# Optimization experiments

Measured on AMD Instinct MI355X. Metric: run time of the kernel, lower is better.

The kernel has to match this reference:

```python
import jax, jax.numpy as jnp
import numpy as np

BETA = 0.99
TOL = 1e-4
MAX_ITER = 1000
EPS = 1e-3
B, N, HF, HV, KV = 65536, 32, 25, 128, 8


def fhat(x, fp):
    W1, b1, W2, b2, W3, b3 = fp
    h = jax.nn.softplus(x @ W1 + b1)
    h = jax.nn.softplus(h @ W2 + b2)
    return h @ W3 + b3  # (B,1,N)


def V(z, vp):
    # Lyapunov function: V(z) = ||g(z)-g(0)||^2 + eps*||z||^2 ; V(0)=0, V>0 elsewhere.
    W1, b1, W2, b2, W3, b3 = vp
    def mlp(u):
        h = jax.nn.softplus(u @ W1 + b1)
        h = jax.nn.softplus(h @ W2 + b2)
        return h @ W3 + b3
    h = mlp(z)
    h0 = mlp(jnp.zeros((1, 1, z.shape[-1]), z.dtype))
    return (jnp.sum((h - h0) ** 2, axis=-1, keepdims=True)
            + EPS * jnp.sum(z * z, axis=-1, keepdims=True))  # (B,1,1)


def newton_F(fhatx, target, gamma, vp):
    # F = gamma - (V(fhatx*gamma)-target)/dV_dgamma  (newton_iter.forward)
    Vg, dV = jax.jvp(lambda g: V(fhatx * g, vp), (gamma,), (jnp.ones_like(gamma),))
    return gamma - (Vg - target) / dV


def solve_gamma(fhatx, target, vp):
    # Vectorized masked Newton + bisection (rootfind_train.forward).
    gamma = jnp.ones((fhatx.shape[0], 1, 1), fhatx.dtype)
    e1 = jnp.zeros_like(gamma)
    e2 = jnp.ones_like(gamma)
    active = (V(fhatx, vp) - target) > 0.0  # samples needing rootfind

    def cond(s):
        return jnp.logical_and(jnp.any(s[3]), s[4] < MAX_ITER)

    def body(s):
        gamma, e1, e2, m, it = s
        # Newton step on active, unconverged samples
        newt = newton_F(fhatx, target, gamma, vp)
        gamma = jnp.where(m, newt, gamma)
        # bisection backup where Newton left [e1,e2] (or produced non-finite)
        m_bisec = m & ((gamma < e1) | (gamma > e2) | ~jnp.isfinite(gamma))
        a = 0.5 * (e1 + e2)
        s_a = jnp.sign(V(fhatx * a, vp) - target)
        s_1 = jnp.sign(V(fhatx * e1, vp) - target)
        s_2 = jnp.sign(V(fhatx * e2, vp) - target)
        e2 = jnp.where(m_bisec & (s_a * s_1 < 0), a, e2)
        e1 = jnp.where(m_bisec & (s_a * s_2 < 0), a, e1)
        gamma = jnp.where(m_bisec, a, gamma)
        m = active & (jnp.abs(V(fhatx * gamma, vp) - target) > TOL)
        return (gamma, e1, e2, m, it + 1)

    gamma = jax.lax.while_loop(cond, body, (gamma, e1, e2, active, jnp.int32(0)))[0]
    return gamma


@jax.jit
def _forward(x, fp, vp):
    fhatx = fhat(x, fp)
    target = BETA * V(x, vp)
    viol = V(fhatx, vp) > target  # these go through rootfind; rest pass through fhat
    gamma = solve_gamma(fhatx, target, vp)
    return jnp.where(viol, fhatx * gamma, fhatx)


def setup_inputs() -> dict:
    key = jax.random.key(0)
    ks = jax.random.split(key, 13)
    def w(k, shape, fan):
        return jax.random.normal(k, shape, jnp.float32) / np.float32(np.sqrt(fan))
    return {
        'x': jax.random.normal(ks[0], (B, 1, N), jnp.float32),
        'f_W1': w(ks[1], (N, HF), N), 'f_b1': jnp.zeros((HF,), jnp.float32),
        'f_W2': w(ks[2], (HF, HF), HF), 'f_b2': jnp.zeros((HF,), jnp.float32),
        'f_W3': w(ks[3], (HF, N), HF), 'f_b3': jnp.zeros((N,), jnp.float32),
        'v_W1': w(ks[4], (N, HV), N), 'v_b1': jnp.zeros((HV,), jnp.float32),
        'v_W2': w(ks[5], (HV, HV), HV), 'v_b2': jnp.zeros((HV,), jnp.float32),
        'v_W3': w(ks[6], (HV, KV), HV), 'v_b3': jnp.zeros((KV,), jnp.float32),
    }


def reference(x, f_W1, f_b1, f_W2, f_b2, f_W3, f_b3,
              v_W1, v_b1, v_W2, v_b2, v_W3, v_b3):
    fp = (f_W1, f_b1, f_W2, f_b2, f_W3, f_b3)
    vp = (v_W1, v_b1, v_W2, v_b2, v_W3, v_b3)
    return _forward(x, fp, vp)
```

## Files before the change

### kernel.cpp

```cpp
#include <hip/hip_runtime.h>
#include <math.h>

#define BETA_C   0.99f
#define TOL_C    1e-4f
#define ACC_C    1e-3f
#define BRK_C    1e-3f
#define FORCE_C  6
#define MAXIT_C  1000
#define EPS_C    1e-3f
#define BN       65536
#define NN       32
#define HFD      25
#define HVD      128
#define KVD      8
#define G        16
#define GPB      16
#define SGPB     16
#define SBLK     256
#define NQBLK    1024

typedef __attribute__((ext_vector_type(8))) short bf16x8;
typedef __attribute__((ext_vector_type(8))) unsigned short u16x8;
typedef __attribute__((ext_vector_type(4))) float f32x4;

__device__ __forceinline__ void wsync() {
    __builtin_amdgcn_wave_barrier();
    __threadfence_block();
    __builtin_amdgcn_wave_barrier();
}

__device__ __forceinline__ float sp_(float x) {
    return fmaxf(x, 0.f) + log1pf(expf(-fabsf(x)));
}
__device__ __forceinline__ float spf_(float x) {
    return fmaxf(x, 0.f) + __logf(1.f + __expf(-fabsf(x)));
}
__device__ __forceinline__ float sgn_(float d) {
    return (d > 0.f) ? 1.f : ((d < 0.f) ? -1.f : 0.f);
}
__device__ __forceinline__ unsigned short f2bf(float f) {
    unsigned int u = __float_as_uint(f);
    u += 0x7FFFu + ((u >> 16) & 1u);
    return (unsigned short)(u >> 16);
}
__device__ __forceinline__ float bf2f(unsigned short u) {
    return __uint_as_float(((unsigned int)u) << 16);
}

__device__ __forceinline__ void aw_st(unsigned short* aw, int row, int col, float v) {
    const int b = (row * 64 + col * 2) ^ ((row & 3) << 4);
    *(unsigned short*)((char*)aw + b) = f2bf(v);
}
__device__ __forceinline__ bf16x8 aw_ld(const unsigned short* aw, int row, int k) {
    const int b = (row * 64 + k * 2) ^ ((row & 3) << 4);
    return *(const bf16x8*)((const char*)aw + b);
}
__device__ __forceinline__ void hw_st(unsigned short* hw, int row, int col, float v) {
    const int b = (row * 256 + col * 2) ^ ((row & 7) << 4);
    *(unsigned short*)((char*)hw + b) = f2bf(v);
}
__device__ __forceinline__ bf16x8 hw_ld(const unsigned short* hw, int row, int k) {
    const int b = (row * 256 + k * 2) ^ ((row & 7) << 4);
    return *(const bf16x8*)((const char*)hw + b);
}

__device__ __forceinline__ void veval2_sec(
    const int gl, const float (&uA)[8], const float (&uB)[8],
    const float gA, const float gB,
    float2* h1q, const float n2A, const float n2B,
    const float (&b1v)[8], const float (&b2v)[8], const float (&d0c)[8],
    const unsigned short* w2L, const unsigned short* w3L,
    float& VA, float& VB)
{
    const int k0 = gl * 8;
#pragma unroll
    for (int j = 0; j < 8; ++j) {
        const float preA = fmaf(gA, uA[j], b1v[j]);
        const float preB = fmaf(gB, uB[j], b1v[j]);
        h1q[k0 + j] = make_float2(spf_(preA), spf_(preB));
    }
    wsync();
    float aA[8], aB[8];
#pragma unroll
    for (int j = 0; j < 8; ++j) { aA[j] = 0.f; aB[j] = 0.f; }
#pragma unroll 4
    for (int k = 0; k < HVD; ++k) {
        const float2 q = h1q[k];
        const u16x8 wv = *(const u16x8*)(w2L + k * HVD + k0);
#pragma unroll
        for (int j = 0; j < 8; ++j) {
            const float w = bf2f(wv[j]);
            aA[j] = fmaf(q.x, w, aA[j]);
            aB[j] = fmaf(q.y, w, aB[j]);
        }
    }
    wsync();
    float oA[KVD], oB[KVD];
#pragma unroll
    for (int c = 0; c < KVD; ++c) { oA[c] = 0.f; oB[c] = 0.f; }
#pragma unroll
    for (int j = 0; j < 8; ++j) {
        const float h2A = spf_(aA[j] + b2v[j]);
        const float h2B = spf_(aB[j] + b2v[j]);
        const u16x8 w3v = *(const u16x8*)(w3L + (k0 + j) * KVD);
#pragma unroll
        for (int c = 0; c < 8; ++c) {
            const float w3 = bf2f(w3v[c]);
            oA[c] = fmaf(h2A, w3, oA[c]);
            oB[c] = fmaf(h2B, w3, oB[c]);
        }
    }
#pragma unroll
    for (int m = 1; m < G; m <<= 1) {
#pragma unroll
        for (int c = 0; c < KVD; ++c) {
            oA[c] += __shfl_xor(oA[c], m);
            oB[c] += __shfl_xor(oB[c], m);
        }
    }
    float vvA = 0.f, vvB = 0.f;
#pragma unroll
    for (int c = 0; c < KVD; ++c) {
        const float eA = oA[c] + d0c[c];
        const float eB = oB[c] + d0c[c];
        vvA = fmaf(eA, eA, vvA);
        vvB = fmaf(eB, eB, vvB);
    }
    VA = vvA + EPS_C * gA * gA * n2A;
    VB = vvB + EPS_C * gB * gB * n2B;
}

__global__ __launch_bounds__(128) void k_h0(
    const float* __restrict__ vb1, const float* __restrict__ vW2,
    const float* __restrict__ vb2, const float* __restrict__ vW3,
    const float* __restrict__ vb3, float* __restrict__ h0g)
{
    __shared__ float h1s[HVD];
    __shared__ float h2s[HVD];
    int j = threadIdx.x;
    h1s[j] = sp_(vb1[j]);
    __syncthreads();
    float a = vb2[j];
    for (int k = 0; k < HVD; ++k) a = fmaf(h1s[k], vW2[k * HVD + j], a);
    h2s[j] = sp_(a);
    __syncthreads();
    if (j < KVD) {
        float acc = vb3[j];
        for (int k = 0; k < HVD; ++k) acc = fmaf(h2s[k], vW3[k * KVD + j], acc);
        h0g[j] = acc;
    }
}

__global__ __launch_bounds__(256) void k_wprep(
    const float* __restrict__ vW1, const float* __restrict__ vW2,
    const float* __restrict__ vW3,
    unsigned short* __restrict__ w1b, unsigned short* __restrict__ w2b,
    unsigned short* __restrict__ w3b,
    unsigned short* __restrict__ w2s, unsigned short* __restrict__ w3s)
{
    const int t = blockIdx.x * 256 + threadIdx.x;
    const int nth = gridDim.x * 256;
    for (int i = t; i < HVD * NN; i += nth) {
        const int col = i >> 5, k = i & 31;
        w1b[i] = f2bf(vW1[k * HVD + col]);
    }
    for (int i = t; i < HVD * HVD; i += nth) {
        const int col = i >> 7, k = i & 127;
        w2b[i] = f2bf(vW2[k * HVD + col]);
    }
    for (int i = t; i < 16 * HVD; i += nth) {
        const int c = i >> 7, k = i & 127;
        w3b[i] = (c < KVD) ? f2bf(vW3[k * KVD + c]) : (unsigned short)0;
    }
    for (int i = t; i < HVD * HVD; i += nth)
        w2s[i] = f2bf(vW2[i]);
    for (int i = t; i < HVD * KVD; i += nth)
        w3s[i] = f2bf(vW3[i]);
}

__global__ __launch_bounds__(256, 4) void k_setup(
    const float* __restrict__ x_g,
    const float* __restrict__ fW1, const float* __restrict__ fb1,
    const float* __restrict__ fW2, const float* __restrict__ fb2,
    const float* __restrict__ fW3, const float* __restrict__ fb3,
    const float* __restrict__ vb1, const float* __restrict__ vb2,
    const float* __restrict__ vb3,
    const unsigned short* __restrict__ w1b,
    const unsigned short* __restrict__ w2b,
    const unsigned short* __restrict__ w3b,
    const float* __restrict__ h0g,
    float* __restrict__ out,
    int* __restrict__ cnt, int* __restrict__ list, float* __restrict__ tgt,
    float* __restrict__ vfb)
{
    __shared__ float2 xs[GPB][NN + 1];
    __shared__ float fh1[GPB][HFD + 1];
    __shared__ float fh2[GPB][HFD + 1];
    __shared__ __align__(16) unsigned short abf[4][16 * 32];
    __shared__ __align__(16) unsigned short hbf[4][16 * HVD];
    __shared__ int wcnt[4];
    __shared__ int bbase;

    const int tid = threadIdx.x;
    const int gi = tid >> 4;
    const int gl = tid & (G - 1);
    const int w  = tid >> 6;
    const int l  = tid & 63;
    const int q  = l >> 4;
    const int cc = l & 15;
    const int sb = (blockIdx.x * GPB + gi) * 2;
    const int s0 = sb, s1 = sb + 1;
    unsigned short* aw = abf[w];
    unsigned short* hw = hbf[w];

    const float xa0 = x_g[(size_t)s0 * NN + gl];
    const float xa1 = x_g[(size_t)s0 * NN + gl + 16];
    const float xb0 = x_g[(size_t)s1 * NN + gl];
    const float xb1 = x_g[(size_t)s1 * NN + gl + 16];
    xs[gi][gl]      = make_float2(xa0, xb0);
    xs[gi][gl + 16] = make_float2(xa1, xb1);
    const int r0 = 4 * q;
    aw_st(aw, r0,     gl,      xa0); aw_st(aw, r0,     gl + 16, xa1);
    aw_st(aw, r0 + 2, gl,      xb0); aw_st(aw, r0 + 2, gl + 16, xb1);
    wsync();

    float fA0, fA1, fB0, fB1;
#pragma unroll
    for (int si = 0; si < 2; ++si) {
        for (int uu = gl; uu < HFD; uu += G) {
            float a = fb1[uu];
#pragma unroll
            for (int i = 0; i < NN; ++i) {
                const float2 xv2 = xs[gi][i];
                const float xv = si ? xv2.y : xv2.x;
                a = fmaf(xv, fW1[i * HFD + uu], a);
            }
            fh1[gi][uu] = spf_(a);
        }
        wsync();
        for (int uu = gl; uu < HFD; uu += G) {
            float a = fb2[uu];
#pragma unroll
            for (int i = 0; i < HFD; ++i)
                a = fmaf(fh1[gi][i], fW2[i * HFD + uu], a);
            fh2[gi][uu] = spf_(a);
        }
        wsync();
        float fo0 = fb3[gl], fo1 = fb3[gl + 16];
#pragma unroll
        for (int i = 0; i < HFD; ++i) {
            const float h = fh2[gi][i];
            fo0 = fmaf(h, fW3[i * NN + gl], fo0);
            fo1 = fmaf(h, fW3[i * NN + gl + 16], fo1);
        }
        const int ss = si ? s1 : s0;
        out[(size_t)ss * NN + gl]      = fo0;
        out[(size_t)ss * NN + gl + 16] = fo1;
        aw_st(aw, r0 + 1 + 2 * si, gl,      fo0);
        aw_st(aw, r0 + 1 + 2 * si, gl + 16, fo1);
        if (si == 0) { fA0 = fo0; fA1 = fo1; } else { fB0 = fo0; fB1 = fo1; }
        wsync();
    }

    float p0 = fmaf(xa0, xa0, xa1 * xa1);
    float p1 = fmaf(fA0, fA0, fA1 * fA1);
    float p2 = fmaf(xb0, xb0, xb1 * xb1);
    float p3 = fmaf(fB0, fB0, fB1 * fB1);
#pragma unroll
    for (int m = 1; m < G; m <<= 1) {
        p0 += __shfl_xor(p0, m); p1 += __shfl_xor(p1, m);
        p2 += __shfl_xor(p2, m); p3 += __shfl_xor(p3, m);
    }

    float b1v[8], b2v[8];
#pragma unroll
    for (int n = 0; n < 8; ++n) {
        b1v[n] = vb1[n * 16 + cc];
        b2v[n] = vb2[n * 16 + cc];
    }

    const int kq = (l >> 4) * 8;
    const f32x4 zf = {0.f, 0.f, 0.f, 0.f};

    const bf16x8 afr = aw_ld(aw, cc, kq);
    f32x4 acc1[8];
#pragma unroll
    for (int n = 0; n < 8; ++n) {
        const bf16x8 bfr = *(const bf16x8*)(w1b + (n * 16 + cc) * 32 + kq);
        acc1[n] = __builtin_amdgcn_mfma_f32_16x16x32_bf16(afr, bfr, zf, 0, 0, 0);
    }
#pragma unroll
    for (int n = 0; n < 8; ++n) {
#pragma unroll
        for (int r = 0; r < 4; ++r)
            hw_st(hw, r0 + r, n * 16 + cc, spf_(acc1[n][r] + b1v[n]));
    }
    wsync();

    f32x4 acc2[8];
#pragma unroll
    for (int n = 0; n < 8; ++n) acc2[n] = zf;
#pragma unroll
    for (int c = 0; c < 4; ++c) {
        const bf16x8 a2f = hw_ld(hw, cc, c * 32 + kq);
#pragma unroll
        for (int n = 0; n < 8; ++n) {
            const bf16x8 b2f = *(const bf16x8*)(w2b + (n * 16 + cc) * HVD + c * 32 + kq);
            acc2[n] = __builtin_amdgcn_mfma_f32_16x16x32_bf16(a2f, b2f, acc2[n], 0, 0, 0);
        }
    }
    wsync();
#pragma unroll
    for (int n = 0; n < 8; ++n) {
#pragma unroll
        for (int r = 0; r < 4; ++r)
            hw_st(hw, r0 + r, n * 16 + cc, spf_(acc2[n][r] + b2v[n]));
    }
    wsync();

    f32x4 acc3 = zf;
#pragma unroll
    for (int c = 0; c < 4; ++c) {
        const bf16x8 a3f = hw_ld(hw, cc, c * 32 + kq);
        const bf16x8 b3f = *(const bf16x8*)(w3b + cc * HVD + c * 32 + kq);
        acc3 = __builtin_amdgcn_mfma_f32_16x16x32_bf16(a3f, b3f, acc3, 0, 0, 0);
    }

    const float d0 = (cc < KVD) ? (vb3[cc] - h0g[cc]) : 0.f;
    float s_[4];
#pragma unroll
    for (int r = 0; r < 4; ++r) {
        const float e = (cc < KVD) ? (acc3[r] + d0) : 0.f;
        s_[r] = e * e;
    }
#pragma unroll
    for (int m = 1; m < G; m <<= 1) {
#pragma unroll
        for (int r = 0; r < 4; ++r) s_[r] += __shfl_xor(s_[r], m);
    }
    const float Vx0 = s_[0] + EPS_C * p0;
    const float Vf0 = s_[1] + EPS_C * p1;
    const float Vx1 = s_[2] + EPS_C * p2;
    const float Vf1 = s_[3] + EPS_C * p3;

    const float t0 = BETA_C * Vx0;
    const float t1 = BETA_C * Vx1;
    const bool act0 = (Vf0 - t0) > 0.f;
    const bool act1 = (Vf1 - t1) > 0.f;

    const bool lead = (gl == 0 && act0) || (gl == 1 && act1);
    unsigned long long bal = __ballot(lead);
    const int lane = threadIdx.x & 63, wv = threadIdx.x >> 6;
    const int rank = __popcll(bal & ((1ull << lane) - 1ull));
    if (lane == 0) wcnt[wv] = __popcll(bal);
    __syncthreads();
    if (threadIdx.x == 0) {
        int tot = 0;
        for (int i = 0; i < 4; ++i) { int c = wcnt[i]; wcnt[i] = tot; tot += c; }
        bbase = atomicAdd(cnt, tot);
    }
    __syncthreads();
    if (lead) {
        const int p = bbase + wcnt[wv] + rank;
        list[p] = (gl == 0) ? s0 : s1;
        tgt[p]  = (gl == 0) ? t0 : t1;
        vfb[p]  = (gl == 0) ? Vf0 : Vf1;
    }
}

__global__ __launch_bounds__(SBLK, 2) void k_solve(
    const float* __restrict__ vW1, const float* __restrict__ vb1,
    const unsigned short* __restrict__ w2s, const float* __restrict__ vb2,
    const unsigned short* __restrict__ w3s, const float* __restrict__ vb3,
    const float* __restrict__ h0g,
    float* __restrict__ out,
    const int* __restrict__ cnt, const int* __restrict__ list,
    const float* __restrict__ tgt, const float* __restrict__ vfb,
    int* __restrict__ qhead)
{
    __shared__ __align__(16) unsigned short w2L[HVD * HVD];
    __shared__ __align__(16) unsigned short w3L[HVD * KVD];
    __shared__ __align__(8) float2 h1s[SGPB][HVD];
    __shared__ __align__(8) float2 fxs[SGPB][NN];

    {
        const uint4* s2 = (const uint4*)w2s;
        uint4* d2 = (uint4*)w2L;
        for (int i = threadIdx.x; i < (HVD * HVD) / 8; i += SBLK) d2[i] = s2[i];
        const uint4* s3 = (const uint4*)w3s;
        uint4* d3 = (uint4*)w3L;
        for (int i = threadIdx.x; i < (HVD * KVD) / 8; i += SBLK) d3[i] = s3[i];
    }
    __syncthreads();

    const int gi = threadIdx.x >> 4;
    const int gl = threadIdx.x & (G - 1);
    const int n  = *cnt;
    float2* h1q = h1s[gi];
    float2* fxr = fxs[gi];
    const int lead = threadIdx.x & 48;

    const int k0 = gl * 8;
    float b1v[8], b2v[8], d0c[8];
    {
        const float4 a = *(const float4*)(vb1 + k0);
        const float4 b = *(const float4*)(vb1 + k0 + 4);
        b1v[0]=a.x; b1v[1]=a.y; b1v[2]=a.z; b1v[3]=a.w;
        b1v[4]=b.x; b1v[5]=b.y; b1v[6]=b.z; b1v[7]=b.w;
        const float4 c = *(const float4*)(vb2 + k0);
        const float4 d = *(const float4*)(vb2 + k0 + 4);
        b2v[0]=c.x; b2v[1]=c.y; b2v[2]=c.z; b2v[3]=c.w;
        b2v[4]=d.x; b2v[5]=d.y; b2v[6]=d.z; b2v[7]=d.w;
#pragma unroll
        for (int cix = 0; cix < KVD; ++cix) d0c[cix] = vb3[cix] - h0g[cix];
    }

    int sA, sB; float tgA, tgB, fA0, fA1, fB0, fB1, n2A, n2B;
    float uA[8], uB[8];
    float gA, e1A, e2A, vA1, vA2, pgA, pvA;
    float gB, e1B, e2B, vB1, vB2, pgB, pvB;
    bool doneA, doneB;
    int itA, itB, obhA, obhB;

    auto grab = [&]() -> bool {
        int v = 0;
        if (gl == 0) v = atomicAdd(qhead, 2);
        v = __shfl(v, lead);
        if (v >= n) return false;
        const bool hasB = (v + 1) < n;
        sA = list[v]; tgA = tgt[v];
        const float vfA = vfb[v];
        float vfB;
        if (hasB) { sB = list[v + 1]; tgB = tgt[v + 1]; vfB = vfb[v + 1]; }
        else      { sB = sA;          tgB = tgA;        vfB = vfA; }
        fA0 = out[(size_t)sA * NN + gl];
        fA1 = out[(size_t)sA * NN + gl + 16];
        fB0 = out[(size_t)sB * NN + gl];
        fB1 = out[(size_t)sB * NN + gl + 16];
        fxr[gl]      = make_float2(fA0, fB0);
        fxr[gl + 16] = make_float2(fA1, fB1);
        wsync();
        n2A = 0.f; n2B = 0.f;
#pragma unroll
        for (int i = 0; i < NN; ++i) {
            const float2 q = fxr[i];
            n2A = fmaf(q.x, q.x, n2A);
            n2B = fmaf(q.y, q.y, n2B);
        }
#pragma unroll
        for (int j = 0; j < 8; ++j) { uA[j] = 0.f; uB[j] = 0.f; }
#pragma unroll
        for (int i = 0; i < NN; ++i) {
            const float2 q = fxr[i];
            const float4 wa = *(const float4*)(vW1 + i * HVD + k0);
            const float4 wb = *(const float4*)(vW1 + i * HVD + k0 + 4);
            uA[0] = fmaf(q.x, wa.x, uA[0]); uA[1] = fmaf(q.x, wa.y, uA[1]);
            uA[2] = fmaf(q.x, wa.z, uA[2]); uA[3] = fmaf(q.x, wa.w, uA[3]);
            uA[4] = fmaf(q.x, wb.x, uA[4]); uA[5] = fmaf(q.x, wb.y, uA[5]);
            uA[6] = fmaf(q.x, wb.z, uA[6]); uA[7] = fmaf(q.x, wb.w, uA[7]);
            uB[0] = fmaf(q.y, wa.x, uB[0]); uB[1] = fmaf(q.y, wa.y, uB[1]);
            uB[2] = fmaf(q.y, wa.z, uB[2]); uB[3] = fmaf(q.y, wa.w, uB[3]);
            uB[4] = fmaf(q.y, wb.x, uB[4]); uB[5] = fmaf(q.y, wb.y, uB[5]);
            uB[6] = fmaf(q.y, wb.z, uB[6]); uB[7] = fmaf(q.y, wb.w, uB[7]);
        }
        gA = sqrtf(tgA / vfA); e1A = 0.f; e2A = 1.f; vA1 = 0.f; vA2 = vfA;
        pgA = 1.f; pvA = vfA;
        gB = sqrtf(tgB / vfB); e1B = 0.f; e2B = 1.f; vB1 = 0.f; vB2 = vfB;
        pgB = 1.f; pvB = vfB;
        doneA = false; itA = 0; obhA = 0;
        doneB = !hasB; itB = 0; obhB = 0;
        return true;
    };
    if (!grab()) return;

    auto step = [&](bool& done, float& gamma, float& pg, float& pv,
                    float& e1, float& e2, float& v_e1, float& v_e2,
                    int& it, int& obh,
                    const float vp, const float target,
                    const int s, const float f0, const float f1) {
        if (done) return;
        if (fabsf(vp - target) <= TOL_C || (e2 - e1) <= BRK_C) {
            out[(size_t)s * NN + gl]      = f0 * gamma;
            out[(size_t)s * NN + gl + 16] = f1 * gamma;
            done = true;
            return;
        }
        const float sa = sgn_(vp - target);
        const float s1 = sgn_(v_e1 - target);
        if (sa * s1 < 0.f) { e2 = gamma; v_e2 = vp; }
        else               { e1 = gamma; v_e1 = vp; }
        ++it;
        const float newt = gamma - (vp - target) * (gamma - pg) / (vp - pv);
        pg = gamma; pv = vp;
        if (it < FORCE_C && newt >= e1 && newt <= e2) {
            if (fabsf(newt - gamma) <= ACC_C) {
                out[(size_t)s * NN + gl]      = f0 * newt;
                out[(size_t)s * NN + gl + 16] = f1 * newt;
                done = true;
                return;
            }
            gamma = newt;
        } else if (newt > e2 && e2 >= 1.0f) {
            if (++obh >= 2) {
                out[(size_t)s * NN + gl]      = f0;
                out[(size_t)s * NN + gl + 16] = f1;
                done = true;
                return;
            }
            gamma = 0.5f * (e1 + e2);
        } else {
            gamma = 0.5f * (e1 + e2);
        }
        if (it >= MAXIT_C) {
            out[(size_t)s * NN + gl]      = f0 * gamma;
            out[(size_t)s * NN + gl + 16] = f1 * gamma;
            done = true;
        }
    };

    for (;;) {
        float vpA, vpB;
        veval2_sec(gl, uA, uB, gA, gB, h1q, n2A, n2B,
                   b1v, b2v, d0c, w2L, w3L, vpA, vpB);
        step(doneA, gA, pgA, pvA, e1A, e2A, vA1, vA2, itA, obhA, vpA, tgA, sA, fA0, fA1);
        step(doneB, gB, pgB, pvB, e1B, e2B, vB1, vB2, itB, obhB, vpB, tgB, sB, fB0, fB1);
        if (doneA && doneB) {
            if (!grab()) break;
        }
    }
}

extern "C" void kernel_launch(void* const* d_in, const int* in_sizes, int n_in,
                              void* d_out, int out_size, void* d_ws, size_t ws_size,
                              hipStream_t stream)
{
    const float* x   = (const float*)d_in[0];
    const float* fW1 = (const float*)d_in[1];
    const float* fb1 = (const float*)d_in[2];
    const float* fW2 = (const float*)d_in[3];
    const float* fb2 = (const float*)d_in[4];
    const float* fW3 = (const float*)d_in[5];
    const float* fb3 = (const float*)d_in[6];
    const float* vW1 = (const float*)d_in[7];
    const float* vb1 = (const float*)d_in[8];
    const float* vW2 = (const float*)d_in[9];
    const float* vb2 = (const float*)d_in[10];
    const float* vW3 = (const float*)d_in[11];
    const float* vb3 = (const float*)d_in[12];
    float* out = (float*)d_out;

    char* ws = (char*)d_ws;
    int*   cnt   = (int*)ws;
    int*   qhead = (int*)(ws + 4);
    float* h0g   = (float*)(ws + 64);
    int*   list  = (int*)(ws + 128);
    float* tgt   = (float*)(ws + 128 + (size_t)BN * 4);
    float* vfb   = (float*)(ws + 128 + (size_t)BN * 8);
    unsigned short* w1b = (unsigned short*)(ws + 128 + (size_t)BN * 12);
    unsigned short* w2b = w1b + HVD * NN;
    unsigned short* w3b = w2b + HVD * HVD;
    unsigned short* w2s = w3b + 16 * HVD;
    unsigned short* w3s = w2s + HVD * HVD;

    hipMemsetAsync(ws, 0, 8, stream);

    hipLaunchKernelGGL(k_h0, dim3(1), dim3(HVD), 0, stream,
                       vb1, vW2, vb2, vW3, vb3, h0g);

    hipLaunchKernelGGL(k_wprep, dim3(32), dim3(256), 0, stream,
                       vW1, vW2, vW3, w1b, w2b, w3b, w2s, w3s);

    hipLaunchKernelGGL(k_setup, dim3(BN / (GPB * 2)), dim3(256), 0, stream,
                       x, fW1, fb1, fW2, fb2, fW3, fb3,
                       vb1, vb2, vb3, w1b, w2b, w3b,
                       h0g, out, cnt, list, tgt, vfb);

    hipLaunchKernelGGL(k_solve, dim3(NQBLK), dim3(SBLK), 0, stream,
                       vW1, vb1, w2s, vb2, w3s, vb3,
                       h0g, out, cnt, list, tgt, vfb, qhead);
}
```

Before: 309.1 us.

## Pack hidden activations as bf16 pairs, drop W3 LDS copy, use shuffles for inputs

The solve kernel now stores layer-1 activations as packed bf16 pairs in a transposed LDS layout, halving that buffer. It also drops the W3 and fx shared-memory copies, reading W3 straight from global memory and broadcasting input features with wave shuffles. The aim is less LDS traffic and footprint, which may allow more resident blocks. The setup kernel fuses its two per-sample f-MLP passes into one loop that handles both samples together, with fewer syncs. Rounding activations to bf16 adds precision loss in the Newton/bisection V evaluations, which could change convergence and iteration counts.

After: 444.4 us. 43.8% more time.

```diff
diff --git a/kernel.cpp b/kernel.cpp
--- a/kernel.cpp
+++ b/kernel.cpp
@@ -67,9 +67,9 @@
 __device__ __forceinline__ void veval2_sec(
     const int gl, const float (&uA)[8], const float (&uB)[8],
     const float gA, const float gB,
-    float2* h1q, const float n2A, const float n2B,
+    unsigned* h1q, const float n2A, const float n2B,
     const float (&b1v)[8], const float (&b2v)[8], const float (&d0c)[8],
-    const unsigned short* w2L, const unsigned short* w3L,
+    const unsigned short* w2L, const unsigned short* __restrict__ w3s,
     float& VA, float& VB)
 {
     const int k0 = gl * 8;
@@ -77,7 +77,9 @@
     for (int j = 0; j < 8; ++j) {
         const float preA = fmaf(gA, uA[j], b1v[j]);
         const float preB = fmaf(gB, uB[j], b1v[j]);
-        h1q[k0 + j] = make_float2(spf_(preA), spf_(preB));
+        const unsigned pa = f2bf(spf_(preA));
+        const unsigned pb = f2bf(spf_(preB));
+        h1q[(j << 4) | gl] = pa | (pb << 16);
     }
     wsync();
     float aA[8], aB[8];
@@ -85,13 +87,15 @@
     for (int j = 0; j < 8; ++j) { aA[j] = 0.f; aB[j] = 0.f; }
 #pragma unroll 4
     for (int k = 0; k < HVD; ++k) {
-        const float2 q = h1q[k];
+        const unsigned hp = h1q[((k & 7) << 4) | (k >> 3)];
+        const float qx = bf2f((unsigned short)(hp & 0xffffu));
+        const float qy = bf2f((unsigned short)(hp >> 16));
         const u16x8 wv = *(const u16x8*)(w2L + k * HVD + k0);
 #pragma unroll
         for (int j = 0; j < 8; ++j) {
             const float w = bf2f(wv[j]);
-            aA[j] = fmaf(q.x, w, aA[j]);
-            aB[j] = fmaf(q.y, w, aB[j]);
+            aA[j] = fmaf(qx, w, aA[j]);
+            aB[j] = fmaf(qy, w, aB[j]);
         }
     }
     wsync();
@@ -102,7 +106,7 @@
     for (int j = 0; j < 8; ++j) {
         const float h2A = spf_(aA[j] + b2v[j]);
         const float h2B = spf_(aB[j] + b2v[j]);
-        const u16x8 w3v = *(const u16x8*)(w3L + (k0 + j) * KVD);
+        const u16x8 w3v = *(const u16x8*)(w3s + (k0 + j) * KVD);
 #pragma unroll
         for (int c = 0; c < 8; ++c) {
             const float w3 = bf2f(w3v[c]);
@@ -194,8 +198,8 @@
     float* __restrict__ vfb)
 {
     __shared__ float2 xs[GPB][NN + 1];
-    __shared__ float fh1[GPB][HFD + 1];
-    __shared__ float fh2[GPB][HFD + 1];
+    __shared__ float2 fh1[GPB][HFD + 1];
+    __shared__ float2 fh2[GPB][HFD + 1];
     __shared__ __align__(16) unsigned short abf[4][16 * 32];
     __shared__ __align__(16) unsigned short hbf[4][16 * HVD];
     __shared__ int wcnt[4];
@@ -225,42 +229,52 @@
     wsync();
 
     float fA0, fA1, fB0, fB1;
-#pragma unroll
-    for (int si = 0; si < 2; ++si) {
-        for (int uu = gl; uu < HFD; uu += G) {
-            float a = fb1[uu];
-#pragma unroll
-            for (int i = 0; i < NN; ++i) {
-                const float2 xv2 = xs[gi][i];
-                const float xv = si ? xv2.y : xv2.x;
-                a = fmaf(xv, fW1[i * HFD + uu], a);
-            }
-            fh1[gi][uu] = spf_(a);
-        }
-        wsync();
-        for (int uu = gl; uu < HFD; uu += G) {
-            float a = fb2[uu];
-#pragma unroll
-            for (int i = 0; i < HFD; ++i)
-                a = fmaf(fh1[gi][i], fW2[i * HFD + uu], a);
-            fh2[gi][uu] = spf_(a);
-        }
-        wsync();
-        float fo0 = fb3[gl], fo1 = fb3[gl + 16];
+    for (int uu = gl; uu < HFD; uu += G) {
+        float a0 = fb1[uu];
+        float a1 = a0;
+#pragma unroll
+        for (int i = 0; i < NN; ++i) {
+            const float2 xv2 = xs[gi][i];
+            const float wv = fW1[i * HFD + uu];
+            a0 = fmaf(xv2.x, wv, a0);
+            a1 = fmaf(xv2.y, wv, a1);
+        }
+        fh1[gi][uu] = make_float2(spf_(a0), spf_(a1));
+    }
+    wsync();
+    for (int uu = gl; uu < HFD; uu += G) {
+        float a0 = fb2[uu];
+        float a1 = a0;
 #pragma unroll
         for (int i = 0; i < HFD; ++i) {
-            const float h = fh2[gi][i];
-            fo0 = fmaf(h, fW3[i * NN + gl], fo0);
-            fo1 = fmaf(h, fW3[i * NN + gl + 16], fo1);
-        }
-        const int ss = si ? s1 : s0;
-        out[(size_t)ss * NN + gl]      = fo0;
-        out[(size_t)ss * NN + gl + 16] = fo1;
-        aw_st(aw, r0 + 1 + 2 * si, gl,      fo0);
-        aw_st(aw, r0 + 1 + 2 * si, gl + 16, fo1);
-        if (si == 0) { fA0 = fo0; fA1 = fo1; } else { fB0 = fo0; fB1 = fo1; }
-        wsync();
-    }
+            const float2 h = fh1[gi][i];
+            const float wv = fW2[i * HFD + uu];
+            a0 = fmaf(h.x, wv, a0);
+            a1 = fmaf(h.y, wv, a1);
+        }
+        fh2[gi][uu] = make_float2(spf_(a0), spf_(a1));
+    }
+    wsync();
+    {
+        float A0 = fb3[gl], A1 = fb3[gl + 16];
+        float B0 = A0,      B1 = A1;
+#pragma unroll
+        for (int i = 0; i < HFD; ++i) {
+            const float2 h = fh2[gi][i];
+            const float wa = fW3[i * NN + gl];
+            const float wb = fW3[i * NN + gl + 16];
+            A0 = fmaf(h.x, wa, A0); A1 = fmaf(h.x, wb, A1);
+            B0 = fmaf(h.y, wa, B0); B1 = fmaf(h.y, wb, B1);
+        }
+        out[(size_t)s0 * NN + gl]      = A0;
+        out[(size_t)s0 * NN + gl + 16] = A1;
+        out[(size_t)s1 * NN + gl]      = B0;
+        out[(size_t)s1 * NN + gl + 16] = B1;
+        aw_st(aw, r0 + 1, gl, A0); aw_st(aw, r0 + 1, gl + 16, A1);
+        aw_st(aw, r0 + 3, gl, B0); aw_st(aw, r0 + 3, gl + 16, B1);
+        fA0 = A0; fA1 = A1; fB0 = B0; fB1 = B1;
+    }
+    wsync();
 
     float p0 = fmaf(xa0, xa0, xa1 * xa1);
     float p1 = fmaf(fA0, fA0, fA1 * fA1);
@@ -379,25 +393,19 @@
     int* __restrict__ qhead)
 {
     __shared__ __align__(16) unsigned short w2L[HVD * HVD];
-    __shared__ __align__(16) unsigned short w3L[HVD * KVD];
-    __shared__ __align__(8) float2 h1s[SGPB][HVD];
-    __shared__ __align__(8) float2 fxs[SGPB][NN];
+    __shared__ unsigned h1s[SGPB][HVD];
 
     {
         const uint4* s2 = (const uint4*)w2s;
         uint4* d2 = (uint4*)w2L;
         for (int i = threadIdx.x; i < (HVD * HVD) / 8; i += SBLK) d2[i] = s2[i];
-        const uint4* s3 = (const uint4*)w3s;
-        uint4* d3 = (uint4*)w3L;
-        for (int i = threadIdx.x; i < (HVD * KVD) / 8; i += SBLK) d3[i] = s3[i];
     }
     __syncthreads();
 
     const int gi = threadIdx.x >> 4;
     const int gl = threadIdx.x & (G - 1);
     const int n  = *cnt;
-    float2* h1q = h1s[gi];
-    float2* fxr = fxs[gi];
+    unsigned* h1q = h1s[gi];
     const int lead = threadIdx.x & 48;
 
     const int k0 = gl * 8;
@@ -437,31 +445,31 @@
         fA1 = out[(size_t)sA * NN + gl + 16];
         fB0 = out[(size_t)sB * NN + gl];
         fB1 = out[(size_t)sB * NN + gl + 16];
-        fxr[gl]      = make_float2(fA0, fB0);
-        fxr[gl + 16] = make_float2(fA1, fB1);
-        wsync();
-        n2A = 0.f; n2B = 0.f;
+        float pa = fmaf(fA0, fA0, fA1 * fA1);
+        float pb = fmaf(fB0, fB0, fB1 * fB1);
+#pragma unroll
+        for (int m = 1; m < G; m <<= 1) {
+            pa += __shfl_xor(pa, m);
+            pb += __shfl_xor(pb, m);
+        }
+        n2A = pa; n2B = pb;
+#pragma unroll
+        for (int j = 0; j < 8; ++j) { uA[j] = 0.f; uB[j] = 0.f; }
 #pragma unroll
         for (int i = 0; i < NN; ++i) {
-            const float2 q = fxr[i];
-            n2A = fmaf(q.x, q.x, n2A);
-            n2B = fmaf(q.y, q.y, n2B);
-        }
-#pragma unroll
-        for (int j = 0; j < 8; ++j) { uA[j] = 0.f; uB[j] = 0.f; }
-#pragma unroll
-        for (int i = 0; i < NN; ++i) {
-            const float2 q = fxr[i];
+            const int src = lead + (i & 15);
+            const float qx = __shfl((i < 16) ? fA0 : fA1, src);
+            const float qy = __shfl((i < 16) ? fB0 : fB1, src);
             const float4 wa = *(const float4*)(vW1 + i * HVD + k0);
             const float4 wb = *(const float4*)(vW1 + i * HVD + k0 + 4);
-            uA[0] = fmaf(q.x, wa.x, uA[0]); uA[1] = fmaf(q.x, wa.y, uA[1]);
-            uA[2] = fmaf(q.x, wa.z, uA[2]); uA[3] = fmaf(q.x, wa.w, uA[3]);
-            uA[4] = fmaf(q.x, wb.x, uA[4]); uA[5] = fmaf(q.x, wb.y, uA[5]);
-            uA[6] = fmaf(q.x, wb.z, uA[6]); uA[7] = fmaf(q.x, wb.w, uA[7]);
-            uB[0] = fmaf(q.y, wa.x, uB[0]); uB[1] = fmaf(q.y, wa.y, uB[1]);
-            uB[2] = fmaf(q.y, wa.z, uB[2]); uB[3] = fmaf(q.y, wa.w, uB[3]);
-            uB[4] = fmaf(q.y, wb.x, uB[4]); uB[5] = fmaf(q.y, wb.y, uB[5]);
-            uB[6] = fmaf(q.y, wb.z, uB[6]); uB[7] = fmaf(q.y, wb.w, uB[7]);
+            uA[0] = fmaf(qx, wa.x, uA[0]); uA[1] = fmaf(qx, wa.y, uA[1]);
+            uA[2] = fmaf(qx, wa.z, uA[2]); uA[3] = fmaf(qx, wa.w, uA[3]);
+            uA[4] = fmaf(qx, wb.x, uA[4]); uA[5] = fmaf(qx, wb.y, uA[5]);
+            uA[6] = fmaf(qx, wb.z, uA[6]); uA[7] = fmaf(qx, wb.w, uA[7]);
+            uB[0] = fmaf(qy, wa.x, uB[0]); uB[1] = fmaf(qy, wa.y, uB[1]);
+            uB[2] = fmaf(qy, wa.z, uB[2]); uB[3] = fmaf(qy, wa.w, uB[3]);
+            uB[4] = fmaf(qy, wb.x, uB[4]); uB[5] = fmaf(qy, wb.y, uB[5]);
+            uB[6] = fmaf(qy, wb.z, uB[6]); uB[7] = fmaf(qy, wb.w, uB[7]);
         }
         gA = sqrtf(tgA / vfA); e1A = 0.f; e2A = 1.f; vA1 = 0.f; vA2 = vfA;
         pgA = 1.f; pvA = vfA;
@@ -521,7 +529,7 @@
     for (;;) {
         float vpA, vpB;
         veval2_sec(gl, uA, uB, gA, gB, h1q, n2A, n2B,
-                   b1v, b2v, d0c, w2L, w3L, vpA, vpB);
+                   b1v, b2v, d0c, w2L, w3s, vpA, vpB);
         step(doneA, gA, pgA, pvA, e1A, e2A, vA1, vA2, itA, obhA, vpA, tgA, sA, fA0, fA1);
         step(doneB, gB, pgB, pvB, e1B, e2B, vB1, vB2, itB, obhB, vpB, tgB, sB, fB0, fB1);
         if (doneA && doneB) {
```
